# Performance work log

Measured on AMD Instinct MI355X. Metric: run time of the kernel, lower is better.

## Reference

```python
import jax, jax.numpy as jnp
import numpy as np

N_NODES = 100000
N_EDGES = 3200000
ALPHA_KCL = 1.0
ALPHA_KVL = 1.0
EPS = 1e-6


def setup_inputs() -> dict:
    key = jax.random.key(0)
    k1, k2, k3, k4 = jax.random.split(key, 4)
    node_features = jax.random.normal(k1, (N_NODES, 4), dtype=jnp.float32)
    edge_index = jax.random.randint(k2, (2, N_EDGES), 0, N_NODES, dtype=jnp.int64)
    edge_logits = jax.random.normal(k3, (N_EDGES,), dtype=jnp.float32)
    edge_params = jax.random.uniform(k4, (N_EDGES, 2), dtype=jnp.float32)
    return {
        "node_features": node_features,
        "edge_index": edge_index,
        "edge_logits": edge_logits,
        "edge_params": edge_params,
    }


def reference(node_features, edge_index, edge_logits, edge_params):
    n_nodes = node_features.shape[0]
    edge_probs = jax.nn.sigmoid(edge_logits)  # [E]
    src = edge_index[0]  # [E]
    dst = edge_index[1]  # [E]
    v = node_features[:, 0]  # [N] voltage column
    # per-edge current: |v_src - v_dst| / (R + X + eps) * prob
    v_diff = jnp.abs(v[src] - v[dst])
    impedance = edge_params[:, 0] + edge_params[:, 1]
    current = v_diff / (impedance + EPS) * edge_probs  # [E]
    # KCL: each edge subtracts its current at src, adds at dst
    node_sum = (
        jax.ops.segment_sum(current, dst, num_segments=n_nodes)
        - jax.ops.segment_sum(current, src, num_segments=n_nodes)
    )  # [N]
    kcl_loss = jnp.mean(node_sum ** 2)
    # KVL (simplified): mean of per-column unbiased variance of edge_params
    kvl_loss = jnp.var(edge_params, axis=0, ddof=1).mean()
    return ALPHA_KCL * kcl_loss + ALPHA_KVL * kvl_loss
```

## Files before the change

### kernel.cpp

```cpp
#include <hip/hip_runtime.h>
#include <math.h>

#define N_NODES 100000
#define N_EDGES 3200000
#define EPS_F 1e-6f

#define GSLICE_N 25000
#define GNSLICE  4
#define GNCHUNK  64
#define GC_PAIRS (N_EDGES / 2 / GNCHUNK)

#define SLICE_N 12500
#define NSLICE  8
#define NCHUNK  32
#define C_PAIRS (N_EDGES / 2 / NCHUNK)

#define NVARB   6250
#define NKCLB   391

#define SRC_OFF   64
#define DST_OFF   (SRC_OFF + N_EDGES)
#define VD_OFF    (DST_OFF + N_EDGES)
#define W_OFF     (VD_OFF + N_EDGES / 2)
#define PART_OFF  (W_OFF + N_EDGES / 2)
#define V_OFF     (PART_OFF + NCHUNK * N_NODES)
#define VARP_OFF  (V_OFF + N_NODES)
#define KCLP_OFF  (VARP_OFF + 4 * NVARB)
#define WS_FLOATS (KCLP_OFF + NKCLB + 64)

__device__ __forceinline__ float wave_reduce(float v) {
    #pragma unroll
    for (int off = 32; off > 0; off >>= 1) v += __shfl_down(v, off, 64);
    return v;
}

__device__ __forceinline__ void fadd_agent(float* p, float v) {
    unsafeAtomicAdd(p, v);
}

__device__ __forceinline__ unsigned short f2bf(float f) {
    unsigned u = __float_as_uint(f);
    unsigned r = ((u >> 16) & 1u) + 0x7FFFu;
    return (unsigned short)((u + r) >> 16);
}
__device__ __forceinline__ float bf2f(unsigned short h) {
    return __uint_as_float(((unsigned)h) << 16);
}

__global__ __launch_bounds__(256) void prep_kernel(
    const float*  __restrict__ nf,
    const void*   __restrict__ eidx,
    const float*  __restrict__ logits,
    const float2* __restrict__ params,
    float*        __restrict__ ws)
{
    __shared__ float red[4][4];
    const int* i32 = (const int*)eidx;

    int any = 0;
    #pragma unroll
    for (int k = 1; k < 32; k += 2) any |= i32[k];
    const bool is32 = (any != 0);

    const int t = blockIdx.x * blockDim.x + threadIdx.x;

    int2 sp, dp;
    if (is32) {
        sp = ((const int2*)i32)[t];
        dp = ((const int2*)(i32 + N_EDGES))[t];
    } else {
        const int4 a = ((const int4*)i32)[t];
        const int4 b = ((const int4*)(i32 + 2 * N_EDGES))[t];
        sp = make_int2(a.x, a.z);
        dp = make_int2(b.x, b.z);
    }
    ((int2*)(ws + SRC_OFF))[t] = sp;
    ((int2*)(ws + DST_OFF))[t] = dp;

    const float4 pp = ((const float4*)params)[t];
    const float2 lg = ((const float2*)logits)[t];
    const float w0 = (1.0f / (1.0f + __expf(-lg.x))) / (pp.x + pp.y + EPS_F);
    const float w1 = (1.0f / (1.0f + __expf(-lg.y))) / (pp.z + pp.w + EPS_F);
    ((unsigned*)(ws + W_OFF))[t] = (unsigned)f2bf(w0) | ((unsigned)f2bf(w1) << 16);

    if (t < N_NODES) ws[V_OFF + t] = nf[t * 4];

    float s0 = pp.x + pp.z;
    float s1 = pp.y + pp.w;
    float q0 = pp.x * pp.x + pp.z * pp.z;
    float q1 = pp.y * pp.y + pp.w * pp.w;

    s0 = wave_reduce(s0); s1 = wave_reduce(s1);
    q0 = wave_reduce(q0); q1 = wave_reduce(q1);

    const int wid = threadIdx.x >> 6;
    if ((threadIdx.x & 63) == 0) {
        red[wid][0] = s0; red[wid][1] = s1; red[wid][2] = q0; red[wid][3] = q1;
    }
    __syncthreads();
    if (threadIdx.x == 0) {
        float4 o;
        o.x = red[0][0] + red[1][0] + red[2][0] + red[3][0];
        o.y = red[0][1] + red[1][1] + red[2][1] + red[3][1];
        o.z = red[0][2] + red[1][2] + red[2][2] + red[3][2];
        o.w = red[0][3] + red[1][3] + red[2][3] + red[3][3];
        ((float4*)(ws + VARP_OFF))[blockIdx.x] = o;
    }
}


__global__ __launch_bounds__(1024) void vgatherS_kernel(float* __restrict__ ws)
{
    __shared__ unsigned short vs_lds[GSLICE_N];

    const int c  = blockIdx.x & (GNCHUNK - 1);
    const int s  = blockIdx.x >> 6;
    const int lo = s * GSLICE_N;

    const float* vtab = ws + V_OFF;
    for (int j = threadIdx.x; j < GSLICE_N; j += 1024) vs_lds[j] = f2bf(vtab[lo + j]);
    __syncthreads();

    const int2*     srcp = (const int2*)(ws + SRC_OFF);
    unsigned short* vd   = (unsigned short*)(ws + VD_OFF);

    const int p0 = c * GC_PAIRS;
    const int p1 = p0 + GC_PAIRS;

    for (int base = p0 + threadIdx.x; base < p1; base += 4096) {
        int2 q4[4];
        #pragma unroll
        for (int k = 0; k < 4; ++k) {
            int p = base + k * 1024;
            p = (p < p1) ? p : (p1 - 1);
            q4[k] = srcp[p];
        }
        #pragma unroll
        for (int k = 0; k < 4; ++k) {
            const int p = base + k * 1024;
            if (p < p1) {
                const unsigned a = (unsigned)(q4[k].x - lo);
                const unsigned b = (unsigned)(q4[k].y - lo);
                if (a < GSLICE_N) vd[2 * p]     = vs_lds[a];
                if (b < GSLICE_N) vd[2 * p + 1] = vs_lds[b];
            }
        }
    }
}

__global__ __launch_bounds__(1024) void vgatherD_kernel(float* __restrict__ ws)
{
    __shared__ unsigned short vs_lds[GSLICE_N];

    const int c  = blockIdx.x & (GNCHUNK - 1);
    const int s  = blockIdx.x >> 6;
    const int lo = s * GSLICE_N;

    const float* vtab = ws + V_OFF;
    for (int j = threadIdx.x; j < GSLICE_N; j += 1024) vs_lds[j] = f2bf(vtab[lo + j]);
    __syncthreads();

    const int2*     dstp = (const int2*)(ws + DST_OFF);
    const unsigned* vdw  = (const unsigned*)(ws + VD_OFF);
    const unsigned* ww   = (const unsigned*)(ws + W_OFF);
    unsigned short* vd   = (unsigned short*)(ws + VD_OFF);

    const int p0 = c * GC_PAIRS;
    const int p1 = p0 + GC_PAIRS;

    for (int base = p0 + threadIdx.x; base < p1; base += 4096) {
        int2     q4[4];
        unsigned v4[4], w4[4];
        #pragma unroll
        for (int k = 0; k < 4; ++k) {
            int p = base + k * 1024;
            p = (p < p1) ? p : (p1 - 1);
            q4[k] = dstp[p];
            v4[k] = vdw[p];
            w4[k] = ww[p];
        }
        #pragma unroll
        for (int k = 0; k < 4; ++k) {
            const int p = base + k * 1024;
            if (p < p1) {
                const unsigned a = (unsigned)(q4[k].x - lo);
                const unsigned b = (unsigned)(q4[k].y - lo);
                if (a < GSLICE_N) {
                    const float cur = fabsf(bf2f((unsigned short)(v4[k] & 0xFFFF)) - bf2f(vs_lds[a]))
                                      * bf2f((unsigned short)(w4[k] & 0xFFFF));
                    vd[2 * p] = f2bf(cur);
                }
                if (b < GSLICE_N) {
                    const float cur = fabsf(bf2f((unsigned short)(v4[k] >> 16)) - bf2f(vs_lds[b]))
                                      * bf2f((unsigned short)(w4[k] >> 16));
                    vd[2 * p + 1] = f2bf(cur);
                }
            }
        }
    }
}

__global__ __launch_bounds__(1024) void scatter_kernel(float* __restrict__ ws)
{
    __shared__ float bins[SLICE_N];

    const int c  = blockIdx.x & (NCHUNK - 1);
    const int s  = blockIdx.x >> 5;
    const int lo = s * SLICE_N;

    for (int j = threadIdx.x; j < SLICE_N; j += 1024) bins[j] = 0.f;
    __syncthreads();

    const int2*     srcp = (const int2*)(ws + SRC_OFF);
    const int2*     dstp = (const int2*)(ws + DST_OFF);
    const unsigned* curw = (const unsigned*)(ws + VD_OFF);

    const int p0 = c * C_PAIRS;
    const int p1 = p0 + C_PAIRS;

    for (int base = p0 + threadIdx.x; base < p1; base += 8192) {
        int2     s8[8], d8[8];
        unsigned u8[8];
        #pragma unroll
        for (int k = 0; k < 8; ++k) {
            int p = base + k * 1024;
            p = (p < p1) ? p : (p1 - 1);
            s8[k] = srcp[p];
            d8[k] = dstp[p];
            u8[k] = curw[p];
        }
        #pragma unroll
        for (int k = 0; k < 8; ++k) {
            const int p = base + k * 1024;
            if (p < p1) {
                const float c0 = bf2f((unsigned short)(u8[k] & 0xFFFF));
                const float c1 = bf2f((unsigned short)(u8[k] >> 16));
                const unsigned s0 = (unsigned)(s8[k].x - lo);
                const unsigned d0 = (unsigned)(d8[k].x - lo);
                const unsigned s1 = (unsigned)(s8[k].y - lo);
                const unsigned d1 = (unsigned)(d8[k].y - lo);
                if (d0 < SLICE_N) atomicAdd(&bins[d0],  c0);
                if (s0 < SLICE_N) atomicAdd(&bins[s0], -c0);
                if (d1 < SLICE_N) atomicAdd(&bins[d1],  c1);
                if (s1 < SLICE_N) atomicAdd(&bins[s1], -c1);
            }
        }
    }
    __syncthreads();

    float* pt = ws + PART_OFF + (size_t)c * N_NODES + lo;
    for (int j = threadIdx.x; j < SLICE_N; j += 1024) pt[j] = bins[j];
}

__global__ __launch_bounds__(256) void kcl_kernel(float* __restrict__ ws)
{
    __shared__ float red[4];
    const int i = blockIdx.x * blockDim.x + threadIdx.x;
    float acc = 0.f;
    if (i < N_NODES) {
        const float* p = ws + PART_OFF + i;
        float s = 0.f;
        #pragma unroll 8
        for (int c = 0; c < NCHUNK; ++c) s += p[(size_t)c * N_NODES];
        acc = s * s;
    }
    acc = wave_reduce(acc);
    if ((threadIdx.x & 63) == 0) red[threadIdx.x >> 6] = acc;
    __syncthreads();
    if (threadIdx.x == 0)
        ws[KCLP_OFF + blockIdx.x] = red[0] + red[1] + red[2] + red[3];
}

__global__ __launch_bounds__(1024) void final_kernel(
    const float* __restrict__ ws, float* __restrict__ out)
{
    __shared__ float red[16][5];
    float s0 = 0.f, s1 = 0.f, q0 = 0.f, q1 = 0.f, k = 0.f;

    const float4* vp = (const float4*)(ws + VARP_OFF);
    for (int i = threadIdx.x; i < NVARB; i += 1024) {
        const float4 v = vp[i];
        s0 += v.x; s1 += v.y; q0 += v.z; q1 += v.w;
    }
    for (int i = threadIdx.x; i < NKCLB; i += 1024) k += ws[KCLP_OFF + i];

    s0 = wave_reduce(s0); s1 = wave_reduce(s1);
    q0 = wave_reduce(q0); q1 = wave_reduce(q1);
    k  = wave_reduce(k);

    const int wid = threadIdx.x >> 6;
    if ((threadIdx.x & 63) == 0) {
        red[wid][0] = s0; red[wid][1] = s1; red[wid][2] = q0;
        red[wid][3] = q1; red[wid][4] = k;
    }
    __syncthreads();
    if (threadIdx.x == 0) {
        float a0 = 0.f, a1 = 0.f, a2 = 0.f, a3 = 0.f, a4 = 0.f;
        #pragma unroll
        for (int w = 0; w < 16; ++w) {
            a0 += red[w][0]; a1 += red[w][1]; a2 += red[w][2];
            a3 += red[w][3]; a4 += red[w][4];
        }
        const float n    = (float)N_EDGES;
        const float var0 = (a2 - a0 * a0 / n) / (n - 1.0f);
        const float var1 = (a3 - a1 * a1 / n) / (n - 1.0f);
        out[0] = a4 / (float)N_NODES + 0.5f * (var0 + var1);
    }
}

#define FB_NODE_OFF 64
__global__ __launch_bounds__(256) void edge_kernel_fb(
    const float*  __restrict__ nf,
    const void*   __restrict__ eidx,
    const float*  __restrict__ logits,
    const float2* __restrict__ params,
    float*        __restrict__ ws)
{
    const int*       i32 = (const int*)eidx;
    const long long* i64 = (const long long*)eidx;
    int any = 0;
    #pragma unroll
    for (int k = 1; k < 32; k += 2) any |= i32[k];
    const bool is32 = (any != 0);

    float* node_sum = ws + FB_NODE_OFF;
    float* acc      = ws + 1;

    float s0 = 0.f, s1 = 0.f, q0 = 0.f, q1 = 0.f;
    const int tid    = blockIdx.x * blockDim.x + threadIdx.x;
    const int stride = gridDim.x * blockDim.x;
    for (int i = tid; i < N_EDGES; i += stride) {
        int src, dst;
        if (is32) { src = i32[i]; dst = i32[N_EDGES + i]; }
        else      { src = (int)i64[i]; dst = (int)i64[N_EDGES + i]; }
        const float2 ep = params[i];
        const float  p  = 1.0f / (1.0f + __expf(-logits[i]));
        const float cur = fabsf(nf[src * 4] - nf[dst * 4]) / (ep.x + ep.y + EPS_F) * p;
        fadd_agent(node_sum + dst,  cur);
        fadd_agent(node_sum + src, -cur);
        s0 += ep.x; s1 += ep.y; q0 += ep.x * ep.x; q1 += ep.y * ep.y;
    }
    s0 = wave_reduce(s0); s1 = wave_reduce(s1);
    q0 = wave_reduce(q0); q1 = wave_reduce(q1);
    if ((threadIdx.x & 63) == 0) {
        fadd_agent(acc + 0, s0); fadd_agent(acc + 1, s1);
        fadd_agent(acc + 2, q0); fadd_agent(acc + 3, q1);
    }
}

__global__ __launch_bounds__(256) void kcl_kernel_fb(float* __restrict__ ws)
{
    const float* node_sum = ws + FB_NODE_OFF;
    float acc = 0.f;
    const int tid    = blockIdx.x * blockDim.x + threadIdx.x;
    const int stride = gridDim.x * blockDim.x;
    for (int i = tid; i < N_NODES; i += stride) {
        const float v = node_sum[i];
        acc += v * v;
    }
    acc = wave_reduce(acc);
    if ((threadIdx.x & 63) == 0) fadd_agent(ws + 5, acc);
}

__global__ void final_kernel_fb(const float* __restrict__ ws, float* __restrict__ out)
{
    const float s0 = ws[1], s1 = ws[2], q0 = ws[3], q1 = ws[4], k = ws[5];
    const float n  = (float)N_EDGES;
    const float var0 = (q0 - s0 * s0 / n) / (n - 1.0f);
    const float var1 = (q1 - s1 * s1 / n) / (n - 1.0f);
    out[0] = k / (float)N_NODES + 0.5f * (var0 + var1);
}

extern "C" void kernel_launch(void* const* d_in, const int* in_sizes, int n_in,
                              void* d_out, int out_size, void* d_ws, size_t ws_size,
                              hipStream_t stream) {
    const float*  nf     = (const float*)d_in[0];
    const void*   eidx   = d_in[1];
    const float*  logits = (const float*)d_in[2];
    const float2* params = (const float2*)d_in[3];
    float* ws  = (float*)d_ws;
    float* out = (float*)d_out;

    const size_t need = (size_t)WS_FLOATS * sizeof(float);

    if (ws_size >= need) {
        prep_kernel<<<NVARB, 256, 0, stream>>>(nf, eidx, logits, params, ws);
        vgatherS_kernel<<<GNCHUNK * GNSLICE, 1024, 0, stream>>>(ws);
        vgatherD_kernel<<<GNCHUNK * GNSLICE, 1024, 0, stream>>>(ws);
        scatter_kernel<<<NCHUNK * NSLICE, 1024, 0, stream>>>(ws);
        kcl_kernel<<<NKCLB, 256, 0, stream>>>(ws);
        final_kernel<<<1, 1024, 0, stream>>>(ws, out);
    } else {
        hipMemsetAsync(d_ws, 0, 256 + (size_t)N_NODES * sizeof(float), stream);
        edge_kernel_fb<<<2048, 256, 0, stream>>>(nf, eidx, logits, params, ws);
        kcl_kernel_fb<<<200, 256, 0, stream>>>(ws);
        final_kernel_fb<<<1, 1, 0, stream>>>(ws, out);
    }
}
```

Measured before the change: 181.4 us.

## Pack src/dst/current into one int4 record and merge gathers into one kernel

The preprocessing kernel now packs each edge pair's 17-bit src and dst indices into a single int4 record. The gather stage writes the bf16 current back into the spare bits of that same record. The two sliced gather kernels become one kernel that caches the first 80000 voltages in LDS as bf16 and reads the rest from global memory. The scatter kernel reads one packed stream instead of three arrays, and uses 3 slices by 64 chunks, 16-deep batching and vectorized zeroing and stores. This reduces global index traffic and the number of redundant slice passes, at the cost of relying on node indices below 2^17 and on bf16 precision for the voltages held in LDS.

```diff
diff --git a/kernel.cpp b/kernel.cpp
--- a/kernel.cpp
+++ b/kernel.cpp
@@ -5,26 +5,24 @@
 #define N_EDGES 3200000
 #define EPS_F 1e-6f
 
-#define GSLICE_N 25000
-#define GNSLICE  4
-#define GNCHUNK  64
-#define GC_PAIRS (N_EDGES / 2 / GNCHUNK)
-
-#define SLICE_N 12500
-#define NSLICE  8
-#define NCHUNK  32
+#define GS_N     80000
+#define GNB      256
+#define GB_PAIRS (N_EDGES / 2 / GNB)
+
+#define SLICE_N 33336
+#define NSLICE  3
+#define NCHUNK  64
 #define C_PAIRS (N_EDGES / 2 / NCHUNK)
+#define SBATCH  16
 
 #define NVARB   6250
 #define NKCLB   391
 
-#define SRC_OFF   64
-#define DST_OFF   (SRC_OFF + N_EDGES)
-#define VD_OFF    (DST_OFF + N_EDGES)
-#define W_OFF     (VD_OFF + N_EDGES / 2)
-#define PART_OFF  (W_OFF + N_EDGES / 2)
-#define V_OFF     (PART_OFF + NCHUNK * N_NODES)
-#define VARP_OFF  (V_OFF + N_NODES)
+#define PK_OFF    64
+#define PART_OFF  (PK_OFF + 2 * N_EDGES)
+#define W_OFF     PART_OFF
+#define V_OFF     (PART_OFF + N_EDGES / 2)
+#define VARP_OFF  (PART_OFF + NCHUNK * N_NODES)
 #define KCLP_OFF  (VARP_OFF + 4 * NVARB)
 #define WS_FLOATS (KCLP_OFF + NKCLB + 64)
 
@@ -74,8 +72,12 @@
         sp = make_int2(a.x, a.z);
         dp = make_int2(b.x, b.z);
     }
-    ((int2*)(ws + SRC_OFF))[t] = sp;
-    ((int2*)(ws + DST_OFF))[t] = dp;
+    int4 pk;
+    pk.x = (int)((unsigned)sp.x | ((unsigned)dp.x << 17));
+    pk.y = (int)(((unsigned)dp.x) >> 15);
+    pk.z = (int)((unsigned)sp.y | ((unsigned)dp.y << 17));
+    pk.w = (int)(((unsigned)dp.y) >> 15);
+    ((int4*)(ws + PK_OFF))[t] = pk;
 
     const float4 pp = ((const float4*)params)[t];
     const float2 lg = ((const float2*)logits)[t];
@@ -108,137 +110,95 @@
     }
 }
 
-
-__global__ __launch_bounds__(1024) void vgatherS_kernel(float* __restrict__ ws)
-{
-    __shared__ unsigned short vs_lds[GSLICE_N];
-
-    const int c  = blockIdx.x & (GNCHUNK - 1);
+__global__ __launch_bounds__(1024) void gather_kernel(float* __restrict__ ws)
+{
+    __shared__ unsigned vlds32[GS_N / 2];
+
+    const float*  vtab = ws + V_OFF;
+    const float2* v2   = (const float2*)vtab;
+    for (int j = threadIdx.x; j < GS_N / 2; j += 1024) {
+        const float2 f = v2[j];
+        vlds32[j] = (unsigned)f2bf(f.x) | ((unsigned)f2bf(f.y) << 16);
+    }
+    __syncthreads();
+    const unsigned short* vl = (const unsigned short*)vlds32;
+
+    int4*           pk = (int4*)(ws + PK_OFF);
+    const unsigned* ww = (const unsigned*)(ws + W_OFF);
+
+    const int p0   = blockIdx.x * GB_PAIRS;
+    const int p1   = p0 + GB_PAIRS;
+    const int base = p0 + (int)threadIdx.x;
+
+    int4     q[8];
+    unsigned wv[8];
+    #pragma unroll
+    for (int k = 0; k < 8; ++k) {
+        int p = base + k * 1024;
+        p = (p < p1) ? p : (p1 - 1);
+        q[k]  = pk[p];
+        wv[k] = ww[p];
+    }
+    #pragma unroll
+    for (int k = 0; k < 8; ++k) {
+        const int p = base + k * 1024;
+        if (p < p1) {
+            const unsigned lo0 = (unsigned)q[k].x, hi0 = (unsigned)q[k].y;
+            const unsigned lo1 = (unsigned)q[k].z, hi1 = (unsigned)q[k].w;
+            const int s0 = (int)(lo0 & 0x1FFFFu);
+            const int d0 = (int)((lo0 >> 17) | ((hi0 & 3u) << 15));
+            const int s1 = (int)(lo1 & 0x1FFFFu);
+            const int d1 = (int)((lo1 >> 17) | ((hi1 & 3u) << 15));
+            const float vs0 = (s0 < GS_N) ? bf2f(vl[s0]) : vtab[s0];
+            const float vd0 = (d0 < GS_N) ? bf2f(vl[d0]) : vtab[d0];
+            const float vs1 = (s1 < GS_N) ? bf2f(vl[s1]) : vtab[s1];
+            const float vd1 = (d1 < GS_N) ? bf2f(vl[d1]) : vtab[d1];
+            const float c0 = fabsf(vs0 - vd0) * bf2f((unsigned short)(wv[k] & 0xFFFF));
+            const float c1 = fabsf(vs1 - vd1) * bf2f((unsigned short)(wv[k] >> 16));
+            q[k].y = (int)((hi0 & 3u) | ((unsigned)f2bf(c0) << 2));
+            q[k].w = (int)((hi1 & 3u) | ((unsigned)f2bf(c1) << 2));
+            pk[p] = q[k];
+        }
+    }
+}
+
+__global__ __launch_bounds__(1024) void scatter_kernel(float* __restrict__ ws)
+{
+    __shared__ float bins[SLICE_N];
+
+    const int c  = blockIdx.x & (NCHUNK - 1);
     const int s  = blockIdx.x >> 6;
-    const int lo = s * GSLICE_N;
-
-    const float* vtab = ws + V_OFF;
-    for (int j = threadIdx.x; j < GSLICE_N; j += 1024) vs_lds[j] = f2bf(vtab[lo + j]);
-    __syncthreads();
-
-    const int2*     srcp = (const int2*)(ws + SRC_OFF);
-    unsigned short* vd   = (unsigned short*)(ws + VD_OFF);
-
-    const int p0 = c * GC_PAIRS;
-    const int p1 = p0 + GC_PAIRS;
-
-    for (int base = p0 + threadIdx.x; base < p1; base += 4096) {
-        int2 q4[4];
+    const unsigned lo = (unsigned)(s * SLICE_N);
+
+    for (int j = threadIdx.x; j < SLICE_N / 4; j += 1024)
+        ((float4*)bins)[j] = make_float4(0.f, 0.f, 0.f, 0.f);
+    __syncthreads();
+
+    const int4* pk = (const int4*)(ws + PK_OFF);
+
+    const int p0 = c * C_PAIRS;
+    const int p1 = p0 + C_PAIRS;
+
+    for (int base = p0 + (int)threadIdx.x; base < p1; base += 1024 * SBATCH) {
+        int4 q[SBATCH];
         #pragma unroll
-        for (int k = 0; k < 4; ++k) {
+        for (int k = 0; k < SBATCH; ++k) {
             int p = base + k * 1024;
             p = (p < p1) ? p : (p1 - 1);
-            q4[k] = srcp[p];
+            q[k] = pk[p];
         }
         #pragma unroll
-        for (int k = 0; k < 4; ++k) {
+        for (int k = 0; k < SBATCH; ++k) {
             const int p = base + k * 1024;
             if (p < p1) {
-                const unsigned a = (unsigned)(q4[k].x - lo);
-                const unsigned b = (unsigned)(q4[k].y - lo);
-                if (a < GSLICE_N) vd[2 * p]     = vs_lds[a];
-                if (b < GSLICE_N) vd[2 * p + 1] = vs_lds[b];
-            }
-        }
-    }
-}
-
-__global__ __launch_bounds__(1024) void vgatherD_kernel(float* __restrict__ ws)
-{
-    __shared__ unsigned short vs_lds[GSLICE_N];
-
-    const int c  = blockIdx.x & (GNCHUNK - 1);
-    const int s  = blockIdx.x >> 6;
-    const int lo = s * GSLICE_N;
-
-    const float* vtab = ws + V_OFF;
-    for (int j = threadIdx.x; j < GSLICE_N; j += 1024) vs_lds[j] = f2bf(vtab[lo + j]);
-    __syncthreads();
-
-    const int2*     dstp = (const int2*)(ws + DST_OFF);
-    const unsigned* vdw  = (const unsigned*)(ws + VD_OFF);
-    const unsigned* ww   = (const unsigned*)(ws + W_OFF);
-    unsigned short* vd   = (unsigned short*)(ws + VD_OFF);
-
-    const int p0 = c * GC_PAIRS;
-    const int p1 = p0 + GC_PAIRS;
-
-    for (int base = p0 + threadIdx.x; base < p1; base += 4096) {
-        int2     q4[4];
-        unsigned v4[4], w4[4];
-        #pragma unroll
-        for (int k = 0; k < 4; ++k) {
-            int p = base + k * 1024;
-            p = (p < p1) ? p : (p1 - 1);
-            q4[k] = dstp[p];
-            v4[k] = vdw[p];
-            w4[k] = ww[p];
-        }
-        #pragma unroll
-        for (int k = 0; k < 4; ++k) {
-            const int p = base + k * 1024;
-            if (p < p1) {
-                const unsigned a = (unsigned)(q4[k].x - lo);
-                const unsigned b = (unsigned)(q4[k].y - lo);
-                if (a < GSLICE_N) {
-                    const float cur = fabsf(bf2f((unsigned short)(v4[k] & 0xFFFF)) - bf2f(vs_lds[a]))
-                                      * bf2f((unsigned short)(w4[k] & 0xFFFF));
-                    vd[2 * p] = f2bf(cur);
-                }
-                if (b < GSLICE_N) {
-                    const float cur = fabsf(bf2f((unsigned short)(v4[k] >> 16)) - bf2f(vs_lds[b]))
-                                      * bf2f((unsigned short)(w4[k] >> 16));
-                    vd[2 * p + 1] = f2bf(cur);
-                }
-            }
-        }
-    }
-}
-
-__global__ __launch_bounds__(1024) void scatter_kernel(float* __restrict__ ws)
-{
-    __shared__ float bins[SLICE_N];
-
-    const int c  = blockIdx.x & (NCHUNK - 1);
-    const int s  = blockIdx.x >> 5;
-    const int lo = s * SLICE_N;
-
-    for (int j = threadIdx.x; j < SLICE_N; j += 1024) bins[j] = 0.f;
-    __syncthreads();
-
-    const int2*     srcp = (const int2*)(ws + SRC_OFF);
-    const int2*     dstp = (const int2*)(ws + DST_OFF);
-    const unsigned* curw = (const unsigned*)(ws + VD_OFF);
-
-    const int p0 = c * C_PAIRS;
-    const int p1 = p0 + C_PAIRS;
-
-    for (int base = p0 + threadIdx.x; base < p1; base += 8192) {
-        int2     s8[8], d8[8];
-        unsigned u8[8];
-        #pragma unroll
-        for (int k = 0; k < 8; ++k) {
-            int p = base + k * 1024;
-            p = (p < p1) ? p : (p1 - 1);
-            s8[k] = srcp[p];
-            d8[k] = dstp[p];
-            u8[k] = curw[p];
-        }
-        #pragma unroll
-        for (int k = 0; k < 8; ++k) {
-            const int p = base + k * 1024;
-            if (p < p1) {
-                const float c0 = bf2f((unsigned short)(u8[k] & 0xFFFF));
-                const float c1 = bf2f((unsigned short)(u8[k] >> 16));
-                const unsigned s0 = (unsigned)(s8[k].x - lo);
-                const unsigned d0 = (unsigned)(d8[k].x - lo);
-                const unsigned s1 = (unsigned)(s8[k].y - lo);
-                const unsigned d1 = (unsigned)(d8[k].y - lo);
+                const unsigned lo0 = (unsigned)q[k].x, hi0 = (unsigned)q[k].y;
+                const unsigned lo1 = (unsigned)q[k].z, hi1 = (unsigned)q[k].w;
+                const unsigned s0 = (lo0 & 0x1FFFFu) - lo;
+                const unsigned d0 = ((lo0 >> 17) | ((hi0 & 3u) << 15)) - lo;
+                const unsigned s1 = (lo1 & 0x1FFFFu) - lo;
+                const unsigned d1 = ((lo1 >> 17) | ((hi1 & 3u) << 15)) - lo;
+                const float c0 = bf2f((unsigned short)((hi0 >> 2) & 0xFFFFu));
+                const float c1 = bf2f((unsigned short)((hi1 >> 2) & 0xFFFFu));
                 if (d0 < SLICE_N) atomicAdd(&bins[d0],  c0);
                 if (s0 < SLICE_N) atomicAdd(&bins[s0], -c0);
                 if (d1 < SLICE_N) atomicAdd(&bins[d1],  c1);
@@ -248,8 +208,10 @@
     }
     __syncthreads();
 
-    float* pt = ws + PART_OFF + (size_t)c * N_NODES + lo;
-    for (int j = threadIdx.x; j < SLICE_N; j += 1024) pt[j] = bins[j];
+    const int n4 = ((int)(N_NODES - lo) < SLICE_N ? (int)(N_NODES - lo) : SLICE_N) / 4;
+    float4* pt4 = (float4*)(ws + PART_OFF + (size_t)c * N_NODES + lo);
+    for (int j = threadIdx.x; j < n4; j += 1024)
+        pt4[j] = ((const float4*)bins)[j];
 }
 
 __global__ __launch_bounds__(256) void kcl_kernel(float* __restrict__ ws)
@@ -385,8 +347,7 @@
 
     if (ws_size >= need) {
         prep_kernel<<<NVARB, 256, 0, stream>>>(nf, eidx, logits, params, ws);
-        vgatherS_kernel<<<GNCHUNK * GNSLICE, 1024, 0, stream>>>(ws);
-        vgatherD_kernel<<<GNCHUNK * GNSLICE, 1024, 0, stream>>>(ws);
+        gather_kernel<<<GNB, 1024, 0, stream>>>(ws);
         scatter_kernel<<<NCHUNK * NSLICE, 1024, 0, stream>>>(ws);
         kcl_kernel<<<NKCLB, 256, 0, stream>>>(ws);
         final_kernel<<<1, 1024, 0, stream>>>(ws, out);
```

Result: no change. 183.9 us (+1.4%).
